# Optimization experiments

Measured on AMD Instinct MI355X. Metric: run time of the kernel, lower is better.

The kernel has to match this reference:

```python
import jax, jax.numpy as jnp
import numpy as np

N_NODES = 100000
N_EDGES = 1600000
D_FEAT = 64


def setup_inputs() -> dict:
    key = jax.random.key(0)
    k1, k2, k3, k4 = jax.random.split(key, 4)
    input = jax.random.normal(k1, (N_NODES, D_FEAT), dtype=jnp.float32)
    edge_weight = jax.random.uniform(k2, (N_EDGES,), dtype=jnp.float32)
    edge_src = jax.random.randint(k3, (N_EDGES,), 0, N_NODES, dtype=jnp.int64)
    edge_dst = jax.random.randint(k4, (N_EDGES,), 0, N_NODES, dtype=jnp.int64)
    return {"input": input, "edge_weight": edge_weight,
            "edge_src": edge_src, "edge_dst": edge_dst}


def reference(input, edge_weight, edge_src, edge_dst):
    # message: gather source node features, scale by edge weight -> (|E|, d)
    message = input[edge_src] * edge_weight[:, None]
    # aggregate: scatter-add edge messages to destination nodes -> (|V|, d)
    update = jax.ops.segment_sum(message, edge_dst, num_segments=input.shape[0])
    # combine: residual combination of input and update
    return input + update
```

## Files before the change

kernel.cpp:

```cpp
#include <hip/hip_runtime.h>
#include <hip/hip_bf16.h>

#define D_FEAT 64
#define NPB 128
#define NPB_SHIFT 7
#define NL1 256
#define MAX_NB 1024
#define SCAN_T 256
#define SCAN_PER_T 8
#define SCAN_CHUNK (SCAN_T * SCAN_PER_T)
#define SRC_BITS 17
#define SRC_MASK 0x1FFFF
#define CVT_BLOCKS 2048
#define W_SCALE 32768.0f
#define W_INV (1.0f / 32768.0f)

typedef unsigned int uint_t;

__device__ inline unsigned short f32_to_bf16_rn(float f) {
    uint_t x = __float_as_uint(f);
    uint_t r = (x + 0x7fffu + ((x >> 16) & 1u)) >> 16;
    return (unsigned short)r;
}

__global__ void mp_pre_kernel(const int* __restrict__ edst,
                              int* __restrict__ counts_T,
                              int n_edges, int nb_buckets,
                              const float2* __restrict__ in2,
                              uint_t* __restrict__ bfrow, int ncvt) {
    __shared__ int hist[MAX_NB];
    int t = threadIdx.x;
    if (blockIdx.x < NL1) {
        for (int k = t; k < nb_buckets; k += blockDim.x) hist[k] = 0;
        __syncthreads();
        int epb = (n_edges + NL1 - 1) / NL1;
        int lo = blockIdx.x * epb;
        int hi = min(n_edges, lo + epb);
        for (int i = lo + t; i < hi; i += blockDim.x)
            atomicAdd(&hist[edst[i] >> NPB_SHIFT], 1);
        __syncthreads();
        for (int k = t; k < nb_buckets; k += blockDim.x)
            counts_T[k * NL1 + blockIdx.x + 1] = hist[k];
        if (blockIdx.x == 0 && t == 0) counts_T[0] = 0;
    } else {
        int g0 = (blockIdx.x - NL1) * blockDim.x + t;
        int stride = CVT_BLOCKS * blockDim.x;
        for (int g = g0; g < ncvt; g += stride) {
            float2 v = in2[g];
            bfrow[g] = (uint_t)f32_to_bf16_rn(v.x) |
                       ((uint_t)f32_to_bf16_rn(v.y) << 16);
        }
    }
}

__global__ void mp_scan1_kernel(int* __restrict__ a, int* __restrict__ partials, int n) {
    __shared__ int tsum[SCAN_T];
    int t = threadIdx.x;
    int base = blockIdx.x * SCAN_CHUNK + t * SCAN_PER_T;
    int v[SCAN_PER_T];
    int s = 0;
    #pragma unroll
    for (int j = 0; j < SCAN_PER_T; ++j) {
        int idx = base + j;
        v[j] = (idx < n) ? a[idx] : 0;
        s += v[j];
    }
    tsum[t] = s;
    __syncthreads();
    #pragma unroll
    for (int off = 1; off < SCAN_T; off <<= 1) {
        int u = (t >= off) ? tsum[t - off] : 0;
        __syncthreads();
        tsum[t] += u;
        __syncthreads();
    }
    if (t == SCAN_T - 1) partials[blockIdx.x] = tsum[t];
    int run = (t == 0) ? 0 : tsum[t - 1];
    #pragma unroll
    for (int j = 0; j < SCAN_PER_T; ++j) {
        int idx = base + j;
        run += v[j];
        if (idx < n) a[idx] = run;
    }
}

__global__ void mp_scan3_kernel(int* __restrict__ a, const int* __restrict__ partials, int n) {
    __shared__ int s[256];
    int b = blockIdx.x;
    if (b == 0) return;
    int t = threadIdx.x;
    s[t] = (t < b) ? partials[t] : 0;
    __syncthreads();
    #pragma unroll
    for (int off = 128; off > 0; off >>= 1) {
        if (t < off) s[t] += s[t + off];
        __syncthreads();
    }
    int add = s[0];
    int base = b * SCAN_CHUNK + t * SCAN_PER_T;
    #pragma unroll
    for (int j = 0; j < SCAN_PER_T; ++j) {
        int idx = base + j;
        if (idx < n) a[idx] += add;
    }
}

__global__ void mp_l1scatter_kernel(const int* __restrict__ esrc,
                                    const int* __restrict__ edst,
                                    const float* __restrict__ ew,
                                    const int* __restrict__ counts_T,
                                    int2* __restrict__ elistA,
                                    int n_edges, int nb_buckets) {
    __shared__ int cur[MAX_NB];
    int t = threadIdx.x;
    for (int k = t; k < nb_buckets; k += blockDim.x)
        cur[k] = counts_T[k * NL1 + blockIdx.x];
    __syncthreads();
    int epb = (n_edges + NL1 - 1) / NL1;
    int lo = blockIdx.x * epb;
    int hi = min(n_edges, lo + epb);
    for (int i = lo + t; i < hi; i += blockDim.x) {
        int d = edst[i];
        int pos = atomicAdd(&cur[d >> NPB_SHIFT], 1);
        elistA[pos] = make_int2(esrc[i] | ((d & (NPB - 1)) << SRC_BITS),
                                __float_as_int(ew[i]));
    }
}

__global__ void mp_l2sort_kernel(const int2* __restrict__ elistA,
                                 const int* __restrict__ counts_T,
                                 uint_t* __restrict__ elistB4,
                                 int* __restrict__ node_start,
                                 int n_nodes, int n_edges, int nb_buckets) {
    __shared__ int nh[NPB];
    __shared__ int cur[NPB];
    int k = blockIdx.x;
    int t = threadIdx.x;
    if (t < NPB) nh[t] = 0;
    __syncthreads();

    int base = counts_T[k * NL1];
    int end  = (k + 1 < nb_buckets) ? counts_T[(k + 1) * NL1] : n_edges;
    int cnt  = end - base;

    for (int i = t; i < cnt; i += 256)
        atomicAdd(&nh[elistA[base + i].x >> SRC_BITS], 1);
    __syncthreads();

    #pragma unroll
    for (int off = 1; off < NPB; off <<= 1) {
        int v = (t < NPB && t >= off) ? nh[t - off] : 0;
        __syncthreads();
        if (t < NPB) nh[t] += v;
        __syncthreads();
    }

    if (t < NPB) {
        int excl = base + ((t == 0) ? 0 : nh[t - 1]);
        cur[t] = excl;
        int g = k * NPB + t;
        if (g < n_nodes) node_start[g] = excl;
    }
    if (k == nb_buckets - 1 && t == 0) node_start[n_nodes] = n_edges;
    __syncthreads();

    for (int i = t; i < cnt; i += 256) {
        int2 r = elistA[base + i];
        int pos = atomicAdd(&cur[r.x >> SRC_BITS], 1);
        int w15 = (int)(__int_as_float(r.y) * W_SCALE + 0.5f);
        w15 = min(32767, max(0, w15));
        elistB4[pos] = (uint_t)(r.x & SRC_MASK) | ((uint_t)w15 << 17);
    }
}

__global__ void mp_cvt_kernel(const float2* __restrict__ in2,
                              uint_t* __restrict__ bfrow, int n) {
    int g = blockIdx.x * blockDim.x + threadIdx.x;
    if (g >= n) return;
    float2 v = in2[g];
    bfrow[g] = (uint_t)f32_to_bf16_rn(v.x) | ((uint_t)f32_to_bf16_rn(v.y) << 16);
}

__global__ void mp_gather3_kernel(const float* __restrict__ input,
                                  const uint_t* __restrict__ bfrow,
                                  const int* __restrict__ node_start,
                                  const uint_t* __restrict__ elist4,
                                  float* __restrict__ out, int n_nodes) {
    int wid = (blockIdx.x * blockDim.x + threadIdx.x) >> 6;
    if (wid >= n_nodes) return;
    int lane = threadIdx.x & 63;
    int h = lane >> 5;
    int l5 = lane & 31;
    int b = node_start[wid];
    int cnt = node_start[wid + 1] - b;

    float ax = 0.0f, ay = 0.0f;
    for (int cbase = 0; cbase < cnt; cbase += 64) {
        int m = min(64, cnt - cbase);
        int rv = (int)elist4[b + cbase + min(lane, m - 1)];
        int jp = 0;
        for (; jp + 16 <= m; jp += 16) {
            int   s[8];
            float w[8];
            uint_t u[8];
            #pragma unroll
            for (int q = 0; q < 8; ++q) {
                uint_t vq = (uint_t)__shfl(rv, jp + 2 * q + h, 64);
                s[q] = (int)(vq & SRC_MASK);
                w[q] = (float)(vq >> 17) * W_INV;
            }
            #pragma unroll
            for (int q = 0; q < 8; ++q)
                u[q] = bfrow[((uint_t)s[q] << 5) + l5];
            #pragma unroll
            for (int q = 0; q < 8; ++q) {
                ax = fmaf(__uint_as_float(u[q] << 16), w[q], ax);
                ay = fmaf(__uint_as_float(u[q] & 0xffff0000u), w[q], ay);
            }
        }
        for (int j = jp; j < m; j += 2) {
            int jj = j + h;
            int jc = (jj < m) ? jj : (m - 1);
            uint_t vq = (uint_t)__shfl(rv, jc, 64);
            int sj = (int)(vq & SRC_MASK);
            float wj = (float)(vq >> 17) * W_INV;
            if (jj >= m) wj = 0.0f;
            uint_t uj = bfrow[((uint_t)sj << 5) + l5];
            ax = fmaf(__uint_as_float(uj << 16), wj, ax);
            ay = fmaf(__uint_as_float(uj & 0xffff0000u), wj, ay);
        }
    }
    ax += __shfl_xor(ax, 32, 64);
    ay += __shfl_xor(ay, 32, 64);
    if (h == 0) {
        float2 inp = ((const float2*)input)[((long long)wid << 5) + l5];
        float2 o;
        o.x = inp.x + ax;
        o.y = inp.y + ay;
        ((float2*)out)[((long long)wid << 5) + l5] = o;
    }
}

__global__ void mp_gather2_kernel(const float* __restrict__ input,
                                  const int* __restrict__ node_start,
                                  const uint_t* __restrict__ elist4,
                                  float* __restrict__ out, int n_nodes) {
    int wid = (blockIdx.x * blockDim.x + threadIdx.x) >> 6;
    if (wid >= n_nodes) return;
    int lane = threadIdx.x & 63;
    int b = node_start[wid], e_end = node_start[wid + 1];
    float acc = input[(long long)wid * D_FEAT + lane];
    for (int i = b; i < e_end; ++i) {
        uint_t r = elist4[i];
        float w = (float)(r >> 17) * W_INV;
        acc += input[(long long)(r & SRC_MASK) * D_FEAT + lane] * w;
    }
    out[(long long)wid * D_FEAT + lane] = acc;
}

__global__ void mp_copy_kernel(const float4* __restrict__ in,
                               float4* __restrict__ out, int n4) {
    int i = blockIdx.x * blockDim.x + threadIdx.x;
    if (i < n4) out[i] = in[i];
}

__global__ void mp_scatter_kernel(const float* __restrict__ input,
                                  const float* __restrict__ ew,
                                  const int* __restrict__ esrc,
                                  const int* __restrict__ edst,
                                  float* __restrict__ out, int n_edges) {
    int tid = blockIdx.x * blockDim.x + threadIdx.x;
    int e = tid >> 6;
    if (e >= n_edges) return;
    int lane = tid & 63;
    float v = input[(long long)esrc[e] * D_FEAT + lane] * ew[e];
    atomicAdd(&out[(long long)edst[e] * D_FEAT + lane], v);
}

extern "C" void kernel_launch(void* const* d_in, const int* in_sizes, int n_in,
                              void* d_out, int out_size, void* d_ws, size_t ws_size,
                              hipStream_t stream) {
    const float* input = (const float*)d_in[0];
    const float* ew    = (const float*)d_in[1];
    const int* esrc    = (const int*)d_in[2];
    const int* edst    = (const int*)d_in[3];
    float* out = (float*)d_out;

    int n_nodes = in_sizes[0] / D_FEAT;
    int n_edges = in_sizes[1];

    int nb_buckets = (n_nodes + NPB - 1) / NPB;
    int n_scan = nb_buckets * NL1 + 1;
    int nbs = (n_scan + SCAN_CHUNK - 1) / SCAN_CHUNK;

    size_t head_ints = (size_t)n_scan + 256 + (size_t)n_nodes + 1;
    size_t elist_off = (head_ints * 4 + 255) & ~(size_t)255;
    size_t elistA_bytes = (size_t)n_edges * 8;
    size_t elistB_bytes = (size_t)n_edges * 4;
    size_t needed_base = elist_off + elistA_bytes + elistB_bytes;
    size_t bf_bytes = (size_t)n_nodes * (D_FEAT * 2);
    size_t needed_ded = needed_base + bf_bytes;

    bool sort_ok = (ws_size >= needed_base) && (nb_buckets <= MAX_NB) &&
                   (n_nodes <= (1 << SRC_BITS)) && (nbs <= 256);
    bool bf_ded = sort_ok && (ws_size >= needed_ded);
    bool bf_ovl = sort_ok && !bf_ded && (bf_bytes <= elistA_bytes);

    if (sort_ok) {
        int* counts_T   = (int*)d_ws;
        int* partials   = counts_T + n_scan;
        int* node_start = partials + 256;
        int2* elistA    = (int2*)((char*)d_ws + elist_off);
        uint_t* elistB4 = (uint_t*)((char*)d_ws + elist_off + elistA_bytes);
        uint_t* bfrow   = bf_ded ? (uint_t*)((char*)d_ws + needed_base)
                                 : (uint_t*)elistA;

        int ncvt = n_nodes * (D_FEAT / 2);
        int pre_grid = NL1 + (bf_ded ? CVT_BLOCKS : 0);
        mp_pre_kernel<<<pre_grid, 256, 0, stream>>>(
            edst, counts_T, n_edges, nb_buckets,
            (const float2*)input, bfrow, bf_ded ? ncvt : 0);
        mp_scan1_kernel<<<nbs, SCAN_T, 0, stream>>>(counts_T, partials, n_scan);
        mp_scan3_kernel<<<nbs, SCAN_T, 0, stream>>>(counts_T, partials, n_scan);
        mp_l1scatter_kernel<<<NL1, 256, 0, stream>>>(esrc, edst, ew, counts_T,
                                                     elistA, n_edges, nb_buckets);
        mp_l2sort_kernel<<<nb_buckets, 256, 0, stream>>>(
            elistA, counts_T, elistB4, node_start, n_nodes, n_edges, nb_buckets);

        long long total = (long long)n_nodes * 64;
        if (bf_ded || bf_ovl) {
            if (bf_ovl)
                mp_cvt_kernel<<<(ncvt + 255) / 256, 256, 0, stream>>>(
                    (const float2*)input, bfrow, ncvt);
            mp_gather3_kernel<<<(int)((total + 255) / 256), 256, 0, stream>>>(
                input, bfrow, node_start, elistB4, out, n_nodes);
        } else {
            mp_gather2_kernel<<<(int)((total + 255) / 256), 256, 0, stream>>>(
                input, node_start, elistB4, out, n_nodes);
        }
    } else {
        int n4 = (n_nodes * D_FEAT) / 4;
        mp_copy_kernel<<<(n4 + 255) / 256, 256, 0, stream>>>(
            (const float4*)input, (float4*)out, n4);
        long long total = (long long)n_edges * 64;
        mp_scatter_kernel<<<(int)((total + 255) / 256), 256, 0, stream>>>(
            input, ew, esrc, edst, out, n_edges);
    }
}
```

Before: 110.4 us.

## Fuse bucket sort into gather and replace two-pass scan with decoupled lookback

Merges the second-level per-node sort and the gather into one kernel. Each block sorts its bucket's edges into LDS and immediately accumulates node outputs, so the sorted edge list is never written to or re-read from global memory. The two scan kernels are also replaced by a single scan in which each block publishes its partial sum and spin-waits on the partials of earlier blocks, removing a launch. The cost is a large LDS footprint (32KB) with 512-thread blocks, which may lower occupancy. The spin-wait scan also assumes earlier blocks are scheduled, and the overflow path for large buckets is slow.

```diff
diff --git a/kernel.cpp b/kernel.cpp
--- a/kernel.cpp
+++ b/kernel.cpp
@@ -14,6 +14,8 @@
 #define CVT_BLOCKS 2048
 #define W_SCALE 32768.0f
 #define W_INV (1.0f / 32768.0f)
+#define SG_T 512
+#define MAX_REC 8192
 
 typedef unsigned int uint_t;
 
@@ -26,11 +28,14 @@
 __global__ void mp_pre_kernel(const int* __restrict__ edst,
                               int* __restrict__ counts_T,
                               int n_edges, int nb_buckets,
+                              int* __restrict__ pub,
                               const float2* __restrict__ in2,
                               uint_t* __restrict__ bfrow, int ncvt) {
     __shared__ int hist[MAX_NB];
     int t = threadIdx.x;
     if (blockIdx.x < NL1) {
+        if (blockIdx.x == 0)
+            for (int i = t; i < 256; i += blockDim.x) pub[i] = 0;
         for (int k = t; k < nb_buckets; k += blockDim.x) hist[k] = 0;
         __syncthreads();
         int epb = (n_edges + NL1 - 1) / NL1;
@@ -53,10 +58,12 @@
     }
 }
 
-__global__ void mp_scan1_kernel(int* __restrict__ a, int* __restrict__ partials, int n) {
+__global__ void mp_scanP_kernel(int* __restrict__ a, int n,
+                                int* __restrict__ pub) {
     __shared__ int tsum[SCAN_T];
-    int t = threadIdx.x;
-    int base = blockIdx.x * SCAN_CHUNK + t * SCAN_PER_T;
+    __shared__ int red[SCAN_T];
+    int t = threadIdx.x, bid = blockIdx.x;
+    int base = bid * SCAN_CHUNK + t * SCAN_PER_T;
     int v[SCAN_PER_T];
     int s = 0;
     #pragma unroll
@@ -74,34 +81,26 @@
         tsum[t] += u;
         __syncthreads();
     }
-    if (t == SCAN_T - 1) partials[blockIdx.x] = tsum[t];
-    int run = (t == 0) ? 0 : tsum[t - 1];
+    if (t == SCAN_T - 1) atomicExch(&pub[bid], tsum[t] + 1);
+    int ls = 0;
+    for (int i = t; i < bid; i += SCAN_T) {
+        int p;
+        while ((p = atomicAdd(&pub[i], 0)) == 0) {}
+        ls += p - 1;
+    }
+    red[t] = ls;
+    __syncthreads();
+    #pragma unroll
+    for (int off = 128; off > 0; off >>= 1) {
+        if (t < off) red[t] += red[t + off];
+        __syncthreads();
+    }
+    int run = red[0] + ((t == 0) ? 0 : tsum[t - 1]);
     #pragma unroll
     for (int j = 0; j < SCAN_PER_T; ++j) {
         int idx = base + j;
         run += v[j];
         if (idx < n) a[idx] = run;
-    }
-}
-
-__global__ void mp_scan3_kernel(int* __restrict__ a, const int* __restrict__ partials, int n) {
-    __shared__ int s[256];
-    int b = blockIdx.x;
-    if (b == 0) return;
-    int t = threadIdx.x;
-    s[t] = (t < b) ? partials[t] : 0;
-    __syncthreads();
-    #pragma unroll
-    for (int off = 128; off > 0; off >>= 1) {
-        if (t < off) s[t] += s[t + off];
-        __syncthreads();
-    }
-    int add = s[0];
-    int base = b * SCAN_CHUNK + t * SCAN_PER_T;
-    #pragma unroll
-    for (int j = 0; j < SCAN_PER_T; ++j) {
-        int idx = base + j;
-        if (idx < n) a[idx] += add;
     }
 }
 
@@ -127,6 +126,119 @@
     }
 }
 
+__global__ void __launch_bounds__(SG_T)
+mp_sortgather_kernel(const float* __restrict__ input,
+                     const uint_t* __restrict__ bfrow,
+                     const int2* __restrict__ elistA,
+                     const int* __restrict__ counts_T,
+                     float* __restrict__ out,
+                     int n_nodes, int n_edges, int nb_buckets) {
+    __shared__ int nh[NPB];
+    __shared__ int cur[NPB];
+    __shared__ uint_t rec[MAX_REC];
+    int k = blockIdx.x;
+    int t = threadIdx.x;
+    int base = counts_T[k * NL1];
+    int end  = (k + 1 < nb_buckets) ? counts_T[(k + 1) * NL1] : n_edges;
+    int cnt  = end - base;
+
+    int wv = t >> 6;
+    int lane = t & 63;
+    int h = lane >> 5, l5 = lane & 31;
+
+    if (cnt <= MAX_REC) {
+        if (t < NPB) nh[t] = 0;
+        __syncthreads();
+        for (int i = t; i < cnt; i += SG_T)
+            atomicAdd(&nh[(elistA[base + i].x >> SRC_BITS) & (NPB - 1)], 1);
+        __syncthreads();
+        #pragma unroll
+        for (int off = 1; off < NPB; off <<= 1) {
+            int v = (t < NPB && t >= off) ? nh[t - off] : 0;
+            __syncthreads();
+            if (t < NPB) nh[t] += v;
+            __syncthreads();
+        }
+        if (t < NPB) cur[t] = (t == 0) ? 0 : nh[t - 1];
+        __syncthreads();
+        for (int i = t; i < cnt; i += SG_T) {
+            int2 r = elistA[base + i];
+            int node = (r.x >> SRC_BITS) & (NPB - 1);
+            int pos = atomicAdd(&cur[node], 1);
+            int w15 = (int)(__int_as_float(r.y) * W_SCALE + 0.5f);
+            w15 = min(32767, max(0, w15));
+            rec[pos] = (uint_t)(r.x & SRC_MASK) | ((uint_t)w15 << 17);
+        }
+        __syncthreads();
+
+        for (int node = wv; node < NPB; node += (SG_T / 64)) {
+            int g = k * NPB + node;
+            if (g >= n_nodes) break;
+            int sb = (node == 0) ? 0 : nh[node - 1];
+            int cn = nh[node] - sb;
+            float ax = 0.0f, ay = 0.0f;
+            int j = 0;
+            for (; j + 16 <= cn; j += 16) {
+                uint_t rr[8], u[8];
+                #pragma unroll
+                for (int q = 0; q < 8; ++q) rr[q] = rec[sb + j + 2 * q + h];
+                #pragma unroll
+                for (int q = 0; q < 8; ++q)
+                    u[q] = bfrow[((rr[q] & SRC_MASK) << 5) + l5];
+                #pragma unroll
+                for (int q = 0; q < 8; ++q) {
+                    float w = (float)(rr[q] >> 17) * W_INV;
+                    ax = fmaf(__uint_as_float(u[q] << 16), w, ax);
+                    ay = fmaf(__uint_as_float(u[q] & 0xffff0000u), w, ay);
+                }
+            }
+            for (; j < cn; j += 2) {
+                int jj = j + h;
+                if (jj < cn) {
+                    uint_t rr = rec[sb + jj];
+                    uint_t u = bfrow[((rr & SRC_MASK) << 5) + l5];
+                    float w = (float)(rr >> 17) * W_INV;
+                    ax = fmaf(__uint_as_float(u << 16), w, ax);
+                    ay = fmaf(__uint_as_float(u & 0xffff0000u), w, ay);
+                }
+            }
+            ax += __shfl_xor(ax, 32, 64);
+            ay += __shfl_xor(ay, 32, 64);
+            if (h == 0) {
+                float2 inp = ((const float2*)input)[((long long)g << 5) + l5];
+                float2 o;
+                o.x = inp.x + ax;
+                o.y = inp.y + ay;
+                ((float2*)out)[((long long)g << 5) + l5] = o;
+            }
+        }
+    } else {
+        for (int node = wv; node < NPB; node += (SG_T / 64)) {
+            int g = k * NPB + node;
+            if (g >= n_nodes) break;
+            float ax = 0.0f, ay = 0.0f;
+            for (int i = h; i < cnt; i += 2) {
+                int2 r = elistA[base + i];
+                if (((r.x >> SRC_BITS) & (NPB - 1)) == node) {
+                    uint_t u = bfrow[(((uint_t)r.x & SRC_MASK) << 5) + l5];
+                    float w = __int_as_float(r.y);
+                    ax = fmaf(__uint_as_float(u << 16), w, ax);
+                    ay = fmaf(__uint_as_float(u & 0xffff0000u), w, ay);
+                }
+            }
+            ax += __shfl_xor(ax, 32, 64);
+            ay += __shfl_xor(ay, 32, 64);
+            if (h == 0) {
+                float2 inp = ((const float2*)input)[((long long)g << 5) + l5];
+                float2 o;
+                o.x = inp.x + ax;
+                o.y = inp.y + ay;
+                ((float2*)out)[((long long)g << 5) + l5] = o;
+            }
+        }
+    }
+}
+
 __global__ void mp_l2sort_kernel(const int2* __restrict__ elistA,
                                  const int* __restrict__ counts_T,
                                  uint_t* __restrict__ elistB4,
@@ -138,15 +250,12 @@
     int t = threadIdx.x;
     if (t < NPB) nh[t] = 0;
     __syncthreads();
-
     int base = counts_T[k * NL1];
     int end  = (k + 1 < nb_buckets) ? counts_T[(k + 1) * NL1] : n_edges;
     int cnt  = end - base;
-
     for (int i = t; i < cnt; i += 256)
         atomicAdd(&nh[elistA[base + i].x >> SRC_BITS], 1);
     __syncthreads();
-
     #pragma unroll
     for (int off = 1; off < NPB; off <<= 1) {
         int v = (t < NPB && t >= off) ? nh[t - off] : 0;
@@ -154,7 +263,6 @@
         if (t < NPB) nh[t] += v;
         __syncthreads();
     }
-
     if (t < NPB) {
         int excl = base + ((t == 0) ? 0 : nh[t - 1]);
         cur[t] = excl;
@@ -163,7 +271,6 @@
     }
     if (k == nb_buckets - 1 && t == 0) node_start[n_nodes] = n_edges;
     __syncthreads();
-
     for (int i = t; i < cnt; i += 256) {
         int2 r = elistA[base + i];
         int pos = atomicAdd(&cur[r.x >> SRC_BITS], 1);
@@ -193,16 +300,13 @@
     int l5 = lane & 31;
     int b = node_start[wid];
     int cnt = node_start[wid + 1] - b;
-
     float ax = 0.0f, ay = 0.0f;
     for (int cbase = 0; cbase < cnt; cbase += 64) {
         int m = min(64, cnt - cbase);
         int rv = (int)elist4[b + cbase + min(lane, m - 1)];
         int jp = 0;
         for (; jp + 16 <= m; jp += 16) {
-            int   s[8];
-            float w[8];
-            uint_t u[8];
+            int s[8]; float w[8]; uint_t u[8];
             #pragma unroll
             for (int q = 0; q < 8; ++q) {
                 uint_t vq = (uint_t)__shfl(rv, jp + 2 * q + h, 64);
@@ -297,31 +401,49 @@
     size_t elist_off = (head_ints * 4 + 255) & ~(size_t)255;
     size_t elistA_bytes = (size_t)n_edges * 8;
     size_t elistB_bytes = (size_t)n_edges * 4;
-    size_t needed_base = elist_off + elistA_bytes + elistB_bytes;
     size_t bf_bytes = (size_t)n_nodes * (D_FEAT * 2);
-    size_t needed_ded = needed_base + bf_bytes;
-
-    bool sort_ok = (ws_size >= needed_base) && (nb_buckets <= MAX_NB) &&
-                   (n_nodes <= (1 << SRC_BITS)) && (nbs <= 256);
-    bool bf_ded = sort_ok && (ws_size >= needed_ded);
-    bool bf_ovl = sort_ok && !bf_ded && (bf_bytes <= elistA_bytes);
-
-    if (sort_ok) {
+
+    size_t needed_fused = elist_off + elistA_bytes + bf_bytes;
+    size_t needed_base  = elist_off + elistA_bytes + elistB_bytes;
+    size_t needed_ded   = needed_base + bf_bytes;
+
+    bool params_ok = (nb_buckets <= MAX_NB) && (n_nodes <= (1 << SRC_BITS)) &&
+                     (nbs <= 256);
+    bool fused_ok = params_ok && (ws_size >= needed_fused);
+    bool sort_ok  = params_ok && (ws_size >= needed_base);
+    bool bf_ded   = sort_ok && (ws_size >= needed_ded);
+    bool bf_ovl   = sort_ok && !bf_ded && (bf_bytes <= elistA_bytes);
+
+    if (fused_ok) {
+        int* counts_T = (int*)d_ws;
+        int* pub      = counts_T + n_scan;
+        int2* elistA  = (int2*)((char*)d_ws + elist_off);
+        uint_t* bfrow = (uint_t*)((char*)d_ws + elist_off + elistA_bytes);
+        int ncvt = n_nodes * (D_FEAT / 2);
+
+        mp_pre_kernel<<<NL1 + CVT_BLOCKS, 256, 0, stream>>>(
+            edst, counts_T, n_edges, nb_buckets, pub,
+            (const float2*)input, bfrow, ncvt);
+        mp_scanP_kernel<<<nbs, SCAN_T, 0, stream>>>(counts_T, n_scan, pub);
+        mp_l1scatter_kernel<<<NL1, 256, 0, stream>>>(esrc, edst, ew, counts_T,
+                                                     elistA, n_edges, nb_buckets);
+        mp_sortgather_kernel<<<nb_buckets, SG_T, 0, stream>>>(
+            input, bfrow, elistA, counts_T, out, n_nodes, n_edges, nb_buckets);
+    } else if (sort_ok) {
         int* counts_T   = (int*)d_ws;
-        int* partials   = counts_T + n_scan;
-        int* node_start = partials + 256;
+        int* pub        = counts_T + n_scan;
+        int* node_start = pub + 256;
         int2* elistA    = (int2*)((char*)d_ws + elist_off);
         uint_t* elistB4 = (uint_t*)((char*)d_ws + elist_off + elistA_bytes);
         uint_t* bfrow   = bf_ded ? (uint_t*)((char*)d_ws + needed_base)
                                  : (uint_t*)elistA;
-
         int ncvt = n_nodes * (D_FEAT / 2);
+
         int pre_grid = NL1 + (bf_ded ? CVT_BLOCKS : 0);
         mp_pre_kernel<<<pre_grid, 256, 0, stream>>>(
-            edst, counts_T, n_edges, nb_buckets,
+            edst, counts_T, n_edges, nb_buckets, pub,
             (const float2*)input, bfrow, bf_ded ? ncvt : 0);
-        mp_scan1_kernel<<<nbs, SCAN_T, 0, stream>>>(counts_T, partials, n_scan);
-        mp_scan3_kernel<<<nbs, SCAN_T, 0, stream>>>(counts_T, partials, n_scan);
+        mp_scanP_kernel<<<nbs, SCAN_T, 0, stream>>>(counts_T, n_scan, pub);
         mp_l1scatter_kernel<<<NL1, 256, 0, stream>>>(esrc, edst, ew, counts_T,
                                                      elistA, n_edges, nb_buckets);
         mp_l2sort_kernel<<<nb_buckets, 256, 0, stream>>>(
```

Measured after the change: 104.5 us. 1.06x faster.
